# Kernel optimization log

Hardware: AMD Instinct MI355X
Metric: run time of the kernel (lower is better)

## Reference

```python
import jax, jax.numpy as jnp
import numpy as np

D_MODEL = 1024
N_HEADS = 16
HEAD_DIM = D_MODEL // N_HEADS  # 64
SEQ = 2048
BATCH = 2


def setup_inputs() -> dict:
    key = jax.random.key(0)
    ks = jax.random.split(key, 12)
    s = 1.0 / np.sqrt(D_MODEL)
    return {
        "query": jax.random.normal(ks[0], (SEQ, BATCH, D_MODEL), jnp.float32),
        "key": jax.random.normal(ks[1], (SEQ, BATCH, D_MODEL), jnp.float32),
        "value": jax.random.normal(ks[2], (SEQ, BATCH, D_MODEL), jnp.float32),
        "Wq": jax.random.normal(ks[3], (D_MODEL, D_MODEL), jnp.float32) * s,
        "bq": jax.random.normal(ks[4], (D_MODEL,), jnp.float32) * s,
        "Wk": jax.random.normal(ks[5], (D_MODEL, D_MODEL), jnp.float32) * s,
        "bk": jax.random.normal(ks[6], (D_MODEL,), jnp.float32) * s,
        "Wv": jax.random.normal(ks[7], (D_MODEL, D_MODEL), jnp.float32) * s,
        "bv": jax.random.normal(ks[8], (D_MODEL,), jnp.float32) * s,
        "Wo": jax.random.normal(ks[9], (D_MODEL, D_MODEL), jnp.float32) * s,
        "bo": jax.random.normal(ks[10], (D_MODEL,), jnp.float32) * s,
    }


def _rope_tables(seq_len):
    # theta_i = 1 / 10000^(2i/head_dim), i in [0, head_dim//2)
    theta = 1.0 / (10000.0 ** (2.0 * jnp.arange(HEAD_DIM // 2, dtype=jnp.float32) / HEAD_DIM))
    pos = jnp.arange(seq_len, dtype=jnp.float32)[:, None, None, None] * theta  # [S,1,1,hd/2]
    return jnp.sin(pos), jnp.cos(pos)


def _apply_rope(t, sin, cos):
    # t: [S, B, H, hd]; NOTE faithful to source: t2 = q1*sin - q2*cos (minus)
    h = HEAD_DIM // 2
    q1, q2 = t[..., :h], t[..., h:]
    return jnp.concatenate([q1 * cos - q2 * sin, q1 * sin - q2 * cos], axis=-1)


def reference(query, key, value, Wq, bq, Wk, bk, Wv, bv, Wo, bo):
    S, B, _ = query.shape
    q = (query @ Wq.T + bq).reshape(S, B, N_HEADS, HEAD_DIM)
    k = (key @ Wk.T + bk).reshape(S, B, N_HEADS, HEAD_DIM)
    v = (value @ Wv.T + bv).reshape(S, B, N_HEADS, HEAD_DIM)
    sin, cos = _rope_tables(S)
    q = _apply_rope(q, sin, cos)
    k = _apply_rope(k, sin, cos)
    # [S,B,H,d] -> [B,H,S,d]
    q = q.transpose(1, 2, 0, 3)
    k = k.transpose(1, 2, 0, 3)
    v = v.transpose(1, 2, 0, 3)
    scale = 1.0 / jnp.sqrt(jnp.float32(HEAD_DIM))
    scores = jnp.einsum("bhqd,bhkd->bhqk", q, k) * scale
    attn = jax.nn.softmax(scores, axis=-1)
    out = jnp.einsum("bhqk,bhkd->bhqd", attn, v)  # [B,H,S,d]
    out = out.transpose(2, 0, 1, 3).reshape(S, B, D_MODEL)
    return out @ Wo.T + bo
```

## Files before the change

### kernel.cpp

```cpp
#include <hip/hip_runtime.h>
#include <hip/hip_bf16.h>
#include <hip/hip_fp16.h>

#define DMODEL 1024
#define NHEADS 16
#define HDIM   64
#define SEQ    2048
#define BATCH  2
#define MROWS  (SEQ*BATCH)

typedef unsigned int u32;
typedef unsigned short u16;
typedef __attribute__((ext_vector_type(8))) short bfrag;
typedef __attribute__((ext_vector_type(8))) _Float16 hfrag;
typedef __attribute__((ext_vector_type(4))) float f32x4;
typedef __attribute__((ext_vector_type(16))) float f32x16;
typedef union { u32 u[4]; bfrag f; } fragu;
typedef union { u32 u[4]; hfrag f; } fragh;

#define LOG2E 1.44269504088896341f

__device__ __forceinline__ u32 f2bf(float x) {
    unsigned u = __float_as_uint(x);
    return (u + 0x7fffu + ((u >> 16) & 1u)) >> 16;
}
__device__ __forceinline__ float bf2f(u32 h) {
    return __uint_as_float(h << 16);
}
__device__ __forceinline__ u32 pk2bf(float a, float b) {
    __hip_bfloat162 t = __float22bfloat162_rn(make_float2(a, b));
    u32 r;
    __builtin_memcpy(&r, &t, 4);
    return r;
}
__device__ __forceinline__ u32 pkf16(float a, float b) {
#if __has_builtin(__builtin_amdgcn_cvt_pkrtz)
    __fp16 __attribute__((ext_vector_type(2))) t = __builtin_amdgcn_cvt_pkrtz(a, b);
    u32 r;
    __builtin_memcpy(&r, &t, 4);
    return r;
#else
    __half2 t = __floats2half2_rn(a, b);
    u32 r;
    __builtin_memcpy(&r, &t, 4);
    return r;
#endif
}
__device__ __forceinline__ float fexp2(float x) {
#if __has_builtin(__builtin_amdgcn_exp2f)
    return __builtin_amdgcn_exp2f(x);
#else
    return exp2f(x);
#endif
}
__device__ __forceinline__ u32 pkhi(u32 u0, u32 u1) {
#if __has_builtin(__builtin_amdgcn_perm)
    return __builtin_amdgcn_perm(u1, u0, 0x07060302u);
#else
    return (u0 >> 16) | (u1 & 0xffff0000u);
#endif
}

__device__ __forceinline__ void gld16(const void* g, void* l) {
    __builtin_amdgcn_global_load_lds(
        (const __attribute__((address_space(1))) unsigned int*)g,
        (__attribute__((address_space(3))) unsigned int*)l, 16, 0, 0);
}


__global__ __launch_bounds__(256) void prep_kernel(
    const float* __restrict__ Wq, const float* __restrict__ Wk,
    const float* __restrict__ Wv, const float* __restrict__ Wo,
    u16* __restrict__ wqb, u16* __restrict__ wkb, u16* __restrict__ wvb,
    u16* __restrict__ wob, float2* __restrict__ tab)
{
    const int y = blockIdx.y;
    if (y == 3) {
        if (blockIdx.x >= 256) return;
        const int e = blockIdx.x * 256 + threadIdx.x;
        const int s = e >> 5, i = e & 31;
        const double th = exp(-(double)i * (9.210340371976184 / 32.0));
        double sn, cs;
        sincos((double)s * th, &sn, &cs);
        tab[e] = make_float2((float)sn, (float)cs);
        return;
    }
    const float* src = (y == 0) ? Wq : (y == 1) ? Wk : (y == 2) ? Wv : Wo;
    u16* dst = (y == 0) ? wqb : (y == 1) ? wkb : (y == 2) ? wvb : wob;
    const bool f16hi = (y < 3);
    const int lane = threadIdx.x & 63;
    const int wv   = threadIdx.x >> 6;
    const int g8   = lane >> 3;
    const int l8   = lane & 7;
    for (int r = 0; r < 2; ++r) {
        const size_t kb = (size_t)blockIdx.x * 8 + (size_t)r * 4 + wv;
        const float4 x4 = *(const float4*)(src + kb * 256 + lane * 4);
        __align__(8) u16 hb[4];
        __align__(8) u16 lb[4];
        const float xs[4] = {x4.x, x4.y, x4.z, x4.w};
        #pragma unroll
        for (int i = 0; i < 4; ++i) {
            if (f16hi) {
                const __half hh = __float2half(xs[i]);
                hb[i] = __half_as_ushort(hh);
                lb[i] = (u16)f2bf(xs[i] - __half2float(hh));
            } else {
                const u32 h = f2bf(xs[i]);
                hb[i] = (u16)h;
                lb[i] = (u16)f2bf(xs[i] - bf2f(h));
            }
        }
        u16* o = dst + kb * 512 + g8 * 64 + l8 * 4;
        *(uint2*)o        = *(const uint2*)hb;
        *(uint2*)(o + 32) = *(const uint2*)lb;
    }
}

__global__ __launch_bounds__(256) void qkv_gemm_kernel(
    const float* __restrict__ query, const float* __restrict__ key,
    const float* __restrict__ value,
    const u16* __restrict__ Wqb, const u16* __restrict__ Wkb,
    const u16* __restrict__ Wvb,
    const float* __restrict__ bq, const float* __restrict__ bk,
    const float* __restrict__ bv, const float2* __restrict__ tab,
    u16* __restrict__ Qh, u16* __restrict__ Ql,
    u16* __restrict__ Kh, u16* __restrict__ Kl,
    u16* __restrict__ VTh)
{
    __shared__ u16 smem16[32768];
    float* sAf = (float*)smem16;
    u16*   sB  = smem16 + 16384;

    const int z  = blockIdx.z;
    const float* Af   = (z == 0) ? query : (z == 1) ? key : value;
    const u16* Wb     = (z == 0) ? Wqb : (z == 1) ? Wkb : Wvb;
    const float* bias = (z == 0) ? bq : (z == 1) ? bk : bv;
    u16* Oh = (z == 0) ? Qh : (z == 1) ? Kh : VTh;
    u16* Ol = (z == 0) ? Ql : (z == 1) ? Kl : nullptr;
    const float rope_scale = (z == 0) ? 0.125f * LOG2E : 1.0f;
    const int mode = (z == 2) ? 1 : 0;

    const int tid   = threadIdx.x;
    const int w     = tid >> 6;
    const int lane  = tid & 63;
    const int lrow  = lane & 15;
    const int lquad = lane >> 4;

    const int id   = blockIdx.x + 16 * blockIdx.y;
    const int xcd  = id & 7;
    const int jj   = id >> 3;
    const int nblk = jj & 7;
    const int mblk = (xcd << 2) | (jj >> 3);
    const int n0   = nblk * 128;
    const int m0   = mblk * 128;

    const int srow8 = lane >> 3;
    const int sch   = (lane & 7) ^ srow8;

    int aoff0[2], aoff1[2];
    #pragma unroll
    for (int mi = 0; mi < 2; ++mi) {
        const int ra = w * 32 + mi * 16 + lrow;
        aoff0[mi] = ra * 32 + (((2 * lquad)     ^ (ra & 7)) << 2);
        aoff1[mi] = ra * 32 + (((2 * lquad + 1) ^ (ra & 7)) << 2);
    }
    int boffh[8], boffl[8];
    #pragma unroll
    for (int ni = 0; ni < 8; ++ni) {
        const int rb = ni * 16 + lrow;
        boffh[ni] = rb * 64 + ((lquad ^ (rb & 7)) << 3);
        boffl[ni] = rb * 64 + (((lquad + 4) ^ (rb & 7)) << 3);
    }

    f32x4 acc[2][8] = {};

    auto stage = [&](int t) {
        const int h = t & 1;
        #pragma unroll
        for (int i = 0; i < 4; ++i) {
            const int slab = w * 4 + i;
            const int row  = slab * 8 + srow8;
            gld16(Af + (size_t)(m0 + row) * 1024 + t * 32 + sch * 4,
                  sAf + h * 4096 + slab * 256);
            gld16(Wb + (size_t)(n0 + row) * 2048 + t * 64 + sch * 8,
                  sB + h * 8192 + slab * 512);
        }
    };

    auto cvtA = [&](const f32x4 a, const f32x4 b, hfrag& a16, bfrag& abf) {
        fragh fh;
        fh.u[0] = pkf16(a[0], a[1]); fh.u[1] = pkf16(a[2], a[3]);
        fh.u[2] = pkf16(b[0], b[1]); fh.u[3] = pkf16(b[2], b[3]);
        fragu fb;
        fb.u[0] = pkhi(__float_as_uint(a[0]), __float_as_uint(a[1]));
        fb.u[1] = pkhi(__float_as_uint(a[2]), __float_as_uint(a[3]));
        fb.u[2] = pkhi(__float_as_uint(b[0]), __float_as_uint(b[1]));
        fb.u[3] = pkhi(__float_as_uint(b[2]), __float_as_uint(b[3]));
        a16 = fh.f; abf = fb.f;
    };

    stage(0);
    for (int t = 0; t < 32; ++t) {
        __syncthreads();
        if (t < 31) stage(t + 1);
        const int h = t & 1;
        const float* sAh_ = sAf + h * 4096;
        const u16*   sBh_ = sB + h * 8192;

        hfrag a16[2];
        bfrag abf[2], bl[8];
        hfrag bh16[8];
        #pragma unroll
        for (int mi = 0; mi < 2; ++mi) {
            const f32x4 a0 = *(const f32x4*)&sAh_[aoff0[mi]];
            const f32x4 a1 = *(const f32x4*)&sAh_[aoff1[mi]];
            cvtA(a0, a1, a16[mi], abf[mi]);
        }
        #pragma unroll
        for (int ni = 0; ni < 8; ++ni) {
            fragh tmp;
            fragu raw;
            raw.f = *(const bfrag*)&sBh_[boffh[ni]];
            tmp.u[0] = raw.u[0]; tmp.u[1] = raw.u[1];
            tmp.u[2] = raw.u[2]; tmp.u[3] = raw.u[3];
            bh16[ni] = tmp.f;
            bl[ni]   = *(const bfrag*)&sBh_[boffl[ni]];
        }

        #pragma unroll
        for (int mi = 0; mi < 2; ++mi)
            #pragma unroll
            for (int ni = 0; ni < 8; ++ni) {
                acc[mi][ni] = __builtin_amdgcn_mfma_f32_16x16x32_f16(a16[mi], bh16[ni], acc[mi][ni], 0, 0, 0);
                acc[mi][ni] = __builtin_amdgcn_mfma_f32_16x16x32_bf16(abf[mi], bl[ni], acc[mi][ni], 0, 0, 0);
            }
    }

    float bn[8];
    #pragma unroll
    for (int ni = 0; ni < 8; ++ni) bn[ni] = bias[n0 + ni * 16 + lrow];

    if (mode == 0) {
        #pragma unroll
        for (int mi = 0; mi < 2; ++mi)
            #pragma unroll
            for (int r = 0; r < 4; ++r) {
                const int mrow = w * 32 + mi * 16 + lquad * 4 + r;
                const int m  = m0 + mrow;
                const int bb = m & 1;
                const int sg = m >> 1;
                #pragma unroll
                for (int hh = 0; hh < 2; ++hh) {
                    const int head = nblk * 2 + hh;
                    const size_t ob = (((size_t)(bb * NHEADS + head) * SEQ) + sg) * HDIM;
                    #pragma unroll
                    for (int ni = 0; ni < 2; ++ni) {
                        const int i = ni * 16 + lrow;
                        const float2 sc = tab[(size_t)sg * 32 + i];
                        const float x1 = acc[mi][hh * 4 + ni][r]     + bn[hh * 4 + ni];
                        const float x2 = acc[mi][hh * 4 + ni + 2][r] + bn[hh * 4 + ni + 2];
                        const float o1 = (x1 * sc.y - x2 * sc.x) * rope_scale;
                        const float o2 = (x1 * sc.x - x2 * sc.y) * rope_scale;
                        const u32 h1 = f2bf(o1);
                        const u32 h2 = f2bf(o2);
                        Oh[ob + i]      = (u16)h1;  Ol[ob + i]      = (u16)f2bf(o1 - bf2f(h1));
                        Oh[ob + i + 32] = (u16)h2;  Ol[ob + i + 32] = (u16)f2bf(o2 - bf2f(h2));
                    }
                }
            }
        return;
    }
    __syncthreads();
    u32* vb = (u32*)smem16;
    for (int p = 0; p < 2; ++p) {
        if (p) __syncthreads();
        #pragma unroll
        for (int mi = 0; mi < 2; ++mi)
            #pragma unroll
            for (int r = 0; r < 4; ++r) {
                const int mrow = w * 32 + mi * 16 + lquad * 4 + r;
                const int bb = mrow & 1;
                const int sl = mrow >> 1;
                if (bb == p) {
                    #pragma unroll
                    for (int ni = 0; ni < 8; ++ni) {
                        const int d = ni * 16 + lrow;
                        vb[d * 65 + sl] = f2bf(acc[mi][ni][r] + bn[ni]);
                    }
                }
            }
        __syncthreads();
        #pragma unroll
        for (int rep = 0; rep < 4; ++rep) {
            const int c  = rep * 256 + tid;
            const int dc = c >> 3;
            const int s8 = c & 7;
            __align__(8) u16 hb[8];
            #pragma unroll
            for (int j = 0; j < 8; ++j)
                hb[j] = (u16)vb[dc * 65 + s8 * 8 + j];
            const int head = nblk * 2 + (dc >> 6);
            const int dd   = dc & 63;
            const size_t orow = ((size_t)(p * NHEADS + head) * HDIM + dd) * SEQ + (m0 >> 1);
            const int blk16 = (s8 >> 1) * 16;
            const int off   = (s8 & 1) * 4;
            *(uint2*)&Oh[orow + blk16 + off]     = *(const uint2*)&hb[0];
            *(uint2*)&Oh[orow + blk16 + 8 + off] = *(const uint2*)&hb[4];
        }
    }
}

template <int NI>
__device__ __forceinline__ void gemm_body(
    int id,
    const u16* __restrict__ Ab, const u16* __restrict__ Wb,
    const float* __restrict__ bias, float* __restrict__ Of,
    u16* smem16)
{
    u16* sA = smem16;
    u16* sB = smem16 + 16384;

    const int tid   = threadIdx.x;
    const int w     = tid >> 6;
    const int lane  = tid & 63;
    const int lrow  = lane & 15;
    const int lquad = lane >> 4;

    const int NBLK = 1024 / (NI * 16);
    const int xcd  = id & 7;
    const int jj   = id >> 3;
    const int nblk = jj & (NBLK - 1);
    const int mblk = (xcd << 2) | (jj / NBLK);
    const int n0   = nblk * NI * 16;
    const int m0   = mblk * 128;

    const int srow8 = lane >> 3;
    const int sch   = (lane & 7) ^ srow8;

    int aoffh[2], aoffl[2], boffh[NI], boffl[NI];
    #pragma unroll
    for (int mi = 0; mi < 2; ++mi) {
        const int ra = w * 32 + mi * 16 + lrow;
        aoffh[mi] = ra * 64 + ((lquad ^ (ra & 7)) << 3);
        aoffl[mi] = ra * 64 + (((lquad + 4) ^ (ra & 7)) << 3);
    }
    #pragma unroll
    for (int ni = 0; ni < NI; ++ni) {
        const int rb = ni * 16 + lrow;
        boffh[ni] = rb * 64 + ((lquad ^ (rb & 7)) << 3);
        boffl[ni] = rb * 64 + (((lquad + 4) ^ (rb & 7)) << 3);
    }

    f32x4 acc[2][NI] = {};

    auto stage = [&](int t) {
        const int h = t & 1;
        #pragma unroll
        for (int i = 0; i < 4; ++i) {
            const int slab = w * 4 + i;
            const int row  = slab * 8 + srow8;
            gld16(Ab + (size_t)(m0 + row) * 2048 + t * 64 + sch * 8,
                  sA + h * 8192 + slab * 512);
        }
        #pragma unroll
        for (int i = 0; i < NI / 2; ++i) {
            const int slab = w * (NI / 2) + i;
            const int row  = slab * 8 + srow8;
            gld16(Wb + (size_t)(n0 + row) * 2048 + t * 64 + sch * 8,
                  sB + h * (NI * 1024) + slab * 512);
        }
    };

    stage(0);
    for (int t = 0; t < 32; ++t) {
        __syncthreads();
        if (t < 31) stage(t + 1);
        const int h = t & 1;
        const u16* sAh_ = sA + h * 8192;
        const u16* sBh_ = sB + h * (NI * 1024);

        bfrag ah[2], al[2], bh[NI], bl[NI];
        #pragma unroll
        for (int mi = 0; mi < 2; ++mi) {
            ah[mi] = *(const bfrag*)&sAh_[aoffh[mi]];
            al[mi] = *(const bfrag*)&sAh_[aoffl[mi]];
        }
        #pragma unroll
        for (int ni = 0; ni < NI; ++ni) {
            bh[ni] = *(const bfrag*)&sBh_[boffh[ni]];
            bl[ni] = *(const bfrag*)&sBh_[boffl[ni]];
        }

        #pragma unroll
        for (int mi = 0; mi < 2; ++mi)
            #pragma unroll
            for (int ni = 0; ni < NI; ++ni) {
                acc[mi][ni] = __builtin_amdgcn_mfma_f32_16x16x32_bf16(ah[mi], bh[ni], acc[mi][ni], 0, 0, 0);
                acc[mi][ni] = __builtin_amdgcn_mfma_f32_16x16x32_bf16(ah[mi], bl[ni], acc[mi][ni], 0, 0, 0);
                acc[mi][ni] = __builtin_amdgcn_mfma_f32_16x16x32_bf16(al[mi], bh[ni], acc[mi][ni], 0, 0, 0);
            }
    }

    float bn[NI];
    #pragma unroll
    for (int ni = 0; ni < NI; ++ni) bn[ni] = bias[n0 + ni * 16 + lrow];

    #pragma unroll
    for (int mi = 0; mi < 2; ++mi)
        #pragma unroll
        for (int r = 0; r < 4; ++r) {
            const int m = m0 + w * 32 + mi * 16 + lquad * 4 + r;
            #pragma unroll
            for (int ni = 0; ni < NI; ++ni)
                Of[(size_t)m * 1024 + n0 + ni * 16 + lrow] = acc[mi][ni][r] + bn[ni];
        }
}

__global__ __launch_bounds__(256) void out_gemm_kernel(
    const u16* __restrict__ Ab, const u16* __restrict__ Wb,
    const float* __restrict__ bias, float* __restrict__ Of)
{
    __shared__ u16 smem16[24576];
    const int id = blockIdx.x + 16 * blockIdx.y;
    gemm_body<4>(id, Ab, Wb, bias, Of, smem16);
}

__global__ __launch_bounds__(256) void attn_mfma_kernel(
    const u16* __restrict__ Qh, const u16* __restrict__ Ql,
    const u16* __restrict__ Kh, const u16* __restrict__ Kl,
    const u16* __restrict__ Vh,
    u16* __restrict__ AOb)
{
    __shared__ u16 sKh[8192], sKl[8192];
    __shared__ u16 sVh[8192];

    const int tid  = threadIdx.x;
    const int w    = tid >> 6;
    const int lane = tid & 63;
    const int l31  = lane & 31;
    const int g    = lane >> 5;

    const int id = blockIdx.x + 16 * blockIdx.y;
    const int jj = id >> 3;
    const int bh = ((id & 7) << 2) | (jj >> 4);
    const int qt = jj & 15;

    const size_t qg = ((size_t)bh * SEQ + qt * 128 + w * 32 + l31) * HDIM + g * 8;
    bfrag qfh[4], qfl[4];
    #pragma unroll
    for (int ks = 0; ks < 4; ++ks) {
        qfh[ks] = *(const bfrag*)&Qh[qg + ks * 16];
        qfl[ks] = *(const bfrag*)&Ql[qg + ks * 16];
    }

    const int srow   = lane >> 3;
    const int schunk = (lane & 7) ^ srow;
    const u16* gsrc = nullptr; u16* lbase = nullptr; size_t istep = 0, ktstep = 0;
    if (w == 0) {
        gsrc = Kh + ((size_t)bh * SEQ + srow) * HDIM + schunk * 8;
        istep = 8 * 64; ktstep = 64 * 64; lbase = sKh;
    } else if (w == 1) {
        gsrc = Kl + ((size_t)bh * SEQ + srow) * HDIM + schunk * 8;
        istep = 8 * 64; ktstep = 64 * 64; lbase = sKl;
    } else if (w == 2) {
        gsrc = Vh + ((size_t)bh * HDIM + srow) * SEQ + schunk * 8;
        istep = 8 * SEQ; ktstep = 64; lbase = sVh;
    }

    int koff[2][4];
    #pragma unroll
    for (int a = 0; a < 2; ++a) {
        const int row = a * 32 + l31;
        #pragma unroll
        for (int c = 0; c < 4; ++c)
            koff[a][c] = row * 64 + (((c * 2 + g) ^ (row & 7)) << 3);
    }

    f32x16 accO[2] = {};
    float l_loc = 0.0f;

    auto stage = [&](int kt) {
        if (w < 3) {
            const u16* gp = gsrc + (size_t)kt * ktstep;
            u16* dst = lbase + (kt & 1) * 4096;
            #pragma unroll
            for (int i = 0; i < 8; ++i)
                gld16(gp + (size_t)i * istep, dst + i * 512);
        }
    };

    stage(0);
    for (int kt = 0; kt < SEQ / 64; ++kt) {
        __syncthreads();
        if (kt < SEQ / 64 - 1) stage(kt + 1);
        const int po = (kt & 1) * 4096;

        f32x16 accS[2] = {};
        #pragma unroll
        for (int kg = 0; kg < 2; ++kg)
            #pragma unroll
            for (int ks = 0; ks < 4; ++ks) {
                const bfrag kh_ = *(const bfrag*)&sKh[po + koff[kg][ks]];
                const bfrag kl_ = *(const bfrag*)&sKl[po + koff[kg][ks]];
                accS[kg] = __builtin_amdgcn_mfma_f32_32x32x16_bf16(kh_, qfh[ks], accS[kg], 0, 0, 0);
                accS[kg] = __builtin_amdgcn_mfma_f32_32x32x16_bf16(kh_, qfl[ks], accS[kg], 0, 0, 0);
                accS[kg] = __builtin_amdgcn_mfma_f32_32x32x16_bf16(kl_, qfh[ks], accS[kg], 0, 0, 0);
            }

        float pv[2][16];
        #pragma unroll
        for (int kg = 0; kg < 2; ++kg)
            #pragma unroll
            for (int r = 0; r < 16; ++r) {
                const float p = fexp2(accS[kg][r]);
                pv[kg][r] = p;
                l_loc += p;
            }

        #pragma unroll
        for (int kp = 0; kp < 4; ++kp) {
            const int kg = kp >> 1;
            const int t8 = (kp & 1) * 8;
            fragu ph;
            #pragma unroll
            for (int j2 = 0; j2 < 4; ++j2)
                ph.u[j2] = pk2bf(pv[kg][t8 + 2 * j2], pv[kg][t8 + 2 * j2 + 1]);
            #pragma unroll
            for (int dt = 0; dt < 2; ++dt) {
                const bfrag vh = *(const bfrag*)&sVh[po + koff[dt][kp]];
                accO[dt] = __builtin_amdgcn_mfma_f32_32x32x16_bf16(vh, ph.f, accO[dt], 0, 0, 0);
            }
        }
    }

    const float inv = 1.0f / (l_loc + __shfl_xor(l_loc, 32));

    const int b = bh >> 4;
    const int h = bh & 15;
    const int sg = qt * 128 + w * 32 + l31;
    const int rm = sg * BATCH + b;
    #pragma unroll
    for (int dt = 0; dt < 2; ++dt)
        #pragma unroll
        for (int rq = 0; rq < 4; ++rq) {
            const int j0 = 8 * rq + 4 * g;
            const int t  = h * 2 + dt;
            __align__(8) u16 hb[4];
            __align__(8) u16 lb[4];
            #pragma unroll
            for (int i2 = 0; i2 < 4; ++i2) {
                const float v = accO[dt][rq * 4 + i2] * inv;
                const u32 hh = f2bf(v);
                hb[i2] = (u16)hh;
                lb[i2] = (u16)f2bf(v - bf2f(hh));
            }
            u16* o = AOb + (size_t)rm * 2048 + t * 64 + j0;
            *(uint2*)o        = *(const uint2*)hb;
            *(uint2*)(o + 32) = *(const uint2*)lb;
        }
}

extern "C" void kernel_launch(void* const* d_in, const int* in_sizes, int n_in,
                              void* d_out, int out_size, void* d_ws, size_t ws_size,
                              hipStream_t stream)
{
    const float* query = (const float*)d_in[0];
    const float* key   = (const float*)d_in[1];
    const float* value = (const float*)d_in[2];
    const float* Wq    = (const float*)d_in[3];
    const float* bq    = (const float*)d_in[4];
    const float* Wk    = (const float*)d_in[5];
    const float* bk    = (const float*)d_in[6];
    const float* Wv    = (const float*)d_in[7];
    const float* bv    = (const float*)d_in[8];
    const float* Wo    = (const float*)d_in[9];
    const float* bo    = (const float*)d_in[10];
    float* out = (float*)d_out;

    char* wsb = (char*)d_ws;
    const size_t MB = 1024 * 1024;
    u16* Wqb = (u16*)(wsb + 0 * MB);
    u16* Wkb = (u16*)(wsb + 4 * MB);
    u16* Wvb = (u16*)(wsb + 8 * MB);
    float2* tab = (float2*)(wsb + 12 * MB);
    u16* Qh  = (u16*)(wsb + 16 * MB); u16* Ql  = (u16*)(wsb + 24 * MB);
    u16* Kh  = (u16*)(wsb + 32 * MB); u16* Kl  = (u16*)(wsb + 40 * MB);
    u16* VTh = (u16*)(wsb + 48 * MB);
    u16* Wob = (u16*)(wsb + 56 * MB);
    u16* AOb = (u16*)(wsb + 0 * MB);

    prep_kernel<<<dim3(512, 5), 256, 0, stream>>>(
        Wq, Wk, Wv, Wo, Wqb, Wkb, Wvb, Wob, tab);
    qkv_gemm_kernel<<<dim3(16, 16, 3), 256, 0, stream>>>(
        query, key, value,
        Wqb, Wkb, Wvb, bq, bk, bv, tab, Qh, Ql, Kh, Kl, VTh);
    attn_mfma_kernel<<<dim3(16, 32), 256, 0, stream>>>(
        Qh, Ql, Kh, Kl, VTh, AOb);
    out_gemm_kernel<<<dim3(16, 32), 256, 0, stream>>>(AOb, Wob, bo, out);
}
```

Before: 281.0 us.

## Split attention over two key halves and merge with a combine kernel

The attention kernel now gets a third grid dimension that splits the key sequence into two halves. Each half writes unnormalized fp32 partial outputs and row sums, using the output buffer as scratch for one half. A new combine kernel adds the partials, normalizes, and writes the hi/lo bf16 pair in place for the output GEMM. The aim is to double the number of attention blocks for better CU occupancy and tail balance, at the cost of an extra launch and extra fp32 global memory traffic.

```diff
diff --git a/kernel.cpp b/kernel.cpp
--- a/kernel.cpp
+++ b/kernel.cpp
@@ -429,7 +429,7 @@
     const u16* __restrict__ Qh, const u16* __restrict__ Ql,
     const u16* __restrict__ Kh, const u16* __restrict__ Kl,
     const u16* __restrict__ Vh,
-    u16* __restrict__ AOb)
+    float* __restrict__ O0, float* __restrict__ O1, float* __restrict__ lsum)
 {
     __shared__ u16 sKh[8192], sKl[8192];
     __shared__ u16 sVh[8192];
@@ -439,6 +439,7 @@
     const int lane = tid & 63;
     const int l31  = lane & 31;
     const int g    = lane >> 5;
+    const int z    = blockIdx.z;
 
     const int id = blockIdx.x + 16 * blockIdx.y;
     const int jj = id >> 3;
@@ -489,10 +490,11 @@
         }
     };
 
-    stage(0);
-    for (int kt = 0; kt < SEQ / 64; ++kt) {
+    const int kt0 = z * 16;
+    stage(kt0);
+    for (int kt = kt0; kt < kt0 + 16; ++kt) {
         __syncthreads();
-        if (kt < SEQ / 64 - 1) stage(kt + 1);
+        if (kt < kt0 + 15) stage(kt + 1);
         const int po = (kt & 1) * 4096;
 
         f32x16 accS[2] = {};
@@ -533,31 +535,63 @@
         }
     }
 
-    const float inv = 1.0f / (l_loc + __shfl_xor(l_loc, 32));
+    const float ls = l_loc + __shfl_xor(l_loc, 32);
 
     const int b = bh >> 4;
     const int h = bh & 15;
     const int sg = qt * 128 + w * 32 + l31;
     const int rm = sg * BATCH + b;
+    if (lane < 32)
+        lsum[(size_t)z * 65536 + (size_t)bh * 2048 + sg] = ls;
+    float* Op = z ? O1 : O0;
     #pragma unroll
     for (int dt = 0; dt < 2; ++dt)
         #pragma unroll
         for (int rq = 0; rq < 4; ++rq) {
-            const int j0 = 8 * rq + 4 * g;
-            const int t  = h * 2 + dt;
-            __align__(8) u16 hb[4];
-            __align__(8) u16 lb[4];
-            #pragma unroll
-            for (int i2 = 0; i2 < 4; ++i2) {
-                const float v = accO[dt][rq * 4 + i2] * inv;
-                const u32 hh = f2bf(v);
-                hb[i2] = (u16)hh;
-                lb[i2] = (u16)f2bf(v - bf2f(hh));
-            }
-            u16* o = AOb + (size_t)rm * 2048 + t * 64 + j0;
-            *(uint2*)o        = *(const uint2*)hb;
-            *(uint2*)(o + 32) = *(const uint2*)lb;
-        }
+            float4 v4;
+            v4.x = accO[dt][rq * 4 + 0];
+            v4.y = accO[dt][rq * 4 + 1];
+            v4.z = accO[dt][rq * 4 + 2];
+            v4.w = accO[dt][rq * 4 + 3];
+            *(float4*)&Op[(size_t)rm * 1024 + (h * 2 + dt) * 32 + 8 * rq + 4 * g] = v4;
+        }
+}
+
+__global__ __launch_bounds__(256) void combine_kernel(
+    float* __restrict__ O0, const float* __restrict__ O1,
+    const float* __restrict__ lsum)
+{
+    const int lane = threadIdx.x & 63;
+    const int wv   = threadIdx.x >> 6;
+    const int g8   = lane >> 3;
+    const int l8   = lane & 7;
+    #pragma unroll
+    for (int r = 0; r < 8; ++r) {
+        const size_t kb = (size_t)blockIdx.x * 32 + (size_t)r * 4 + wv;
+        const int rm = (int)(kb >> 2);
+        const int t  = ((int)kb & 3) * 8 + g8;
+        const int b  = rm & 1;
+        const int sg = rm >> 1;
+        const int h  = t >> 1;
+        const float l0 = lsum[(size_t)(b * 16 + h) * 2048 + sg];
+        const float l1 = lsum[65536 + (size_t)(b * 16 + h) * 2048 + sg];
+        const float inv = 1.0f / (l0 + l1);
+        const float4 x0 = *(const float4*)(O0 + kb * 256 + lane * 4);
+        const float4 x1 = *(const float4*)(O1 + kb * 256 + lane * 4);
+        const float xs[4] = {x0.x + x1.x, x0.y + x1.y, x0.z + x1.z, x0.w + x1.w};
+        __align__(8) u16 hb[4];
+        __align__(8) u16 lb[4];
+        #pragma unroll
+        for (int i = 0; i < 4; ++i) {
+            const float v = xs[i] * inv;
+            const u32 hh = f2bf(v);
+            hb[i] = (u16)hh;
+            lb[i] = (u16)f2bf(v - bf2f(hh));
+        }
+        u16* o = (u16*)O0 + kb * 512 + g8 * 64 + l8 * 4;
+        *(uint2*)o        = *(const uint2*)hb;
+        *(uint2*)(o + 32) = *(const uint2*)lb;
+    }
 }
 
 extern "C" void kernel_launch(void* const* d_in, const int* in_sizes, int n_in,
@@ -587,14 +621,17 @@
     u16* Kh  = (u16*)(wsb + 32 * MB); u16* Kl  = (u16*)(wsb + 40 * MB);
     u16* VTh = (u16*)(wsb + 48 * MB);
     u16* Wob = (u16*)(wsb + 56 * MB);
-    u16* AOb = (u16*)(wsb + 0 * MB);
+    float* O0   = (float*)(wsb + 0 * MB);
+    float* O1   = out;
+    float* lsum = (float*)(wsb + 60 * MB);
 
     prep_kernel<<<dim3(512, 5), 256, 0, stream>>>(
         Wq, Wk, Wv, Wo, Wqb, Wkb, Wvb, Wob, tab);
     qkv_gemm_kernel<<<dim3(16, 16, 3), 256, 0, stream>>>(
         query, key, value,
         Wqb, Wkb, Wvb, bq, bk, bv, tab, Qh, Ql, Kh, Kl, VTh);
-    attn_mfma_kernel<<<dim3(16, 32), 256, 0, stream>>>(
-        Qh, Ql, Kh, Kl, VTh, AOb);
-    out_gemm_kernel<<<dim3(16, 32), 256, 0, stream>>>(AOb, Wob, bo, out);
-}
+    attn_mfma_kernel<<<dim3(16, 32, 2), 256, 0, stream>>>(
+        Qh, Ql, Kh, Kl, VTh, O0, O1, lsum);
+    combine_kernel<<<dim3(512), 256, 0, stream>>>(O0, O1, lsum);
+    out_gemm_kernel<<<dim3(16, 32), 256, 0, stream>>>((const u16*)O0, Wob, bo, out);
+}
```

New measurement: 288.4 us. 2.6% more time.

## Use fp16-hi/bf16 split to cut MFMA count in QK^T and output GEMM

Applied to the files above, without the earlier changes.

Switches the Q/K split format to an fp16 high part plus a bf16 residual, and the attention output and Wo weights to an fp16 high part plus a bf16 part. This lets the QK^T and output projection use two MFMAs per tile instead of three. For Q (z==0) the low part becomes a plain bf16 of the value rather than a residual, so one product approximates the cross term. The gemm_body template is also inlined into out_gemm_kernel. This trades some precision (fp16 range and the changed residual scheme) for fewer matrix instructions.

```diff
diff --git a/kernel.cpp b/kernel.cpp
--- a/kernel.cpp
+++ b/kernel.cpp
@@ -15,8 +15,7 @@
 typedef __attribute__((ext_vector_type(8))) _Float16 hfrag;
 typedef __attribute__((ext_vector_type(4))) float f32x4;
 typedef __attribute__((ext_vector_type(16))) float f32x16;
-typedef union { u32 u[4]; bfrag f; } fragu;
-typedef union { u32 u[4]; hfrag f; } fragh;
+typedef union { u32 u[4]; bfrag f; hfrag h; } fragu;
 
 #define LOG2E 1.44269504088896341f
 
@@ -87,7 +86,6 @@
     }
     const float* src = (y == 0) ? Wq : (y == 1) ? Wk : (y == 2) ? Wv : Wo;
     u16* dst = (y == 0) ? wqb : (y == 1) ? wkb : (y == 2) ? wvb : wob;
-    const bool f16hi = (y < 3);
     const int lane = threadIdx.x & 63;
     const int wv   = threadIdx.x >> 6;
     const int g8   = lane >> 3;
@@ -100,15 +98,9 @@
         const float xs[4] = {x4.x, x4.y, x4.z, x4.w};
         #pragma unroll
         for (int i = 0; i < 4; ++i) {
-            if (f16hi) {
-                const __half hh = __float2half(xs[i]);
-                hb[i] = __half_as_ushort(hh);
-                lb[i] = (u16)f2bf(xs[i] - __half2float(hh));
-            } else {
-                const u32 h = f2bf(xs[i]);
-                hb[i] = (u16)h;
-                lb[i] = (u16)f2bf(xs[i] - bf2f(h));
-            }
+            const __half hh = __float2half(xs[i]);
+            hb[i] = __half_as_ushort(hh);
+            lb[i] = (u16)f2bf(xs[i] - __half2float(hh));
         }
         u16* o = dst + kb * 512 + g8 * 64 + l8 * 4;
         *(uint2*)o        = *(const uint2*)hb;
@@ -188,15 +180,14 @@
     };
 
     auto cvtA = [&](const f32x4 a, const f32x4 b, hfrag& a16, bfrag& abf) {
-        fragh fh;
+        fragu fh, fb;
         fh.u[0] = pkf16(a[0], a[1]); fh.u[1] = pkf16(a[2], a[3]);
         fh.u[2] = pkf16(b[0], b[1]); fh.u[3] = pkf16(b[2], b[3]);
-        fragu fb;
         fb.u[0] = pkhi(__float_as_uint(a[0]), __float_as_uint(a[1]));
         fb.u[1] = pkhi(__float_as_uint(a[2]), __float_as_uint(a[3]));
         fb.u[2] = pkhi(__float_as_uint(b[0]), __float_as_uint(b[1]));
         fb.u[3] = pkhi(__float_as_uint(b[2]), __float_as_uint(b[3]));
-        a16 = fh.f; abf = fb.f;
+        a16 = fh.h; abf = fb.f;
     };
 
     stage(0);
@@ -218,12 +209,9 @@
         }
         #pragma unroll
         for (int ni = 0; ni < 8; ++ni) {
-            fragh tmp;
             fragu raw;
             raw.f = *(const bfrag*)&sBh_[boffh[ni]];
-            tmp.u[0] = raw.u[0]; tmp.u[1] = raw.u[1];
-            tmp.u[2] = raw.u[2]; tmp.u[3] = raw.u[3];
-            bh16[ni] = tmp.f;
+            bh16[ni] = raw.h;
             bl[ni]   = *(const bfrag*)&sBh_[boffl[ni]];
         }
 
@@ -261,10 +249,17 @@
                         const float x2 = acc[mi][hh * 4 + ni + 2][r] + bn[hh * 4 + ni + 2];
                         const float o1 = (x1 * sc.y - x2 * sc.x) * rope_scale;
                         const float o2 = (x1 * sc.x - x2 * sc.y) * rope_scale;
-                        const u32 h1 = f2bf(o1);
-                        const u32 h2 = f2bf(o2);
-                        Oh[ob + i]      = (u16)h1;  Ol[ob + i]      = (u16)f2bf(o1 - bf2f(h1));
-                        Oh[ob + i + 32] = (u16)h2;  Ol[ob + i + 32] = (u16)f2bf(o2 - bf2f(h2));
+                        const __half h1 = __float2half(o1);
+                        const __half h2 = __float2half(o2);
+                        Oh[ob + i]      = __half_as_ushort(h1);
+                        Oh[ob + i + 32] = __half_as_ushort(h2);
+                        if (z == 0) {
+                            Ol[ob + i]      = (u16)f2bf(o1);
+                            Ol[ob + i + 32] = (u16)f2bf(o2);
+                        } else {
+                            Ol[ob + i]      = (u16)f2bf(o1 - __half2float(h1));
+                            Ol[ob + i + 32] = (u16)f2bf(o2 - __half2float(h2));
+                        }
                     }
                 }
             }
@@ -310,15 +305,15 @@
     }
 }
 
-template <int NI>
-__device__ __forceinline__ void gemm_body(
-    int id,
+__global__ __launch_bounds__(256) void out_gemm_kernel(
     const u16* __restrict__ Ab, const u16* __restrict__ Wb,
-    const float* __restrict__ bias, float* __restrict__ Of,
-    u16* smem16)
+    const float* __restrict__ bias, float* __restrict__ Of)
 {
+    __shared__ u16 smem16[24576];
     u16* sA = smem16;
     u16* sB = smem16 + 16384;
+
+    const int id = blockIdx.x + 16 * blockIdx.y;
 
     const int tid   = threadIdx.x;
     const int w     = tid >> 6;
@@ -326,18 +321,17 @@
     const int lrow  = lane & 15;
     const int lquad = lane >> 4;
 
-    const int NBLK = 1024 / (NI * 16);
     const int xcd  = id & 7;
     const int jj   = id >> 3;
-    const int nblk = jj & (NBLK - 1);
-    const int mblk = (xcd << 2) | (jj / NBLK);
-    const int n0   = nblk * NI * 16;
+    const int nblk = jj & 15;
+    const int mblk = (xcd << 2) | (jj >> 4);
+    const int n0   = nblk * 64;
     const int m0   = mblk * 128;
 
     const int srow8 = lane >> 3;
     const int sch   = (lane & 7) ^ srow8;
 
-    int aoffh[2], aoffl[2], boffh[NI], boffl[NI];
+    int aoffh[2], aoffl[2], boffh[4], boffl[4];
     #pragma unroll
     for (int mi = 0; mi < 2; ++mi) {
         const int ra = w * 32 + mi * 16 + lrow;
@@ -345,13 +339,13 @@
         aoffl[mi] = ra * 64 + (((lquad + 4) ^ (ra & 7)) << 3);
     }
     #pragma unroll
-    for (int ni = 0; ni < NI; ++ni) {
+    for (int ni = 0; ni < 4; ++ni) {
         const int rb = ni * 16 + lrow;
         boffh[ni] = rb * 64 + ((lquad ^ (rb & 7)) << 3);
         boffl[ni] = rb * 64 + (((lquad + 4) ^ (rb & 7)) << 3);
     }
 
-    f32x4 acc[2][NI] = {};
+    f32x4 acc[2][4] = {};
 
     auto stage = [&](int t) {
         const int h = t & 1;
@@ -363,11 +357,11 @@
                   sA + h * 8192 + slab * 512);
         }
         #pragma unroll
-        for (int i = 0; i < NI / 2; ++i) {
-            const int slab = w * (NI / 2) + i;
+        for (int i = 0; i < 2; ++i) {
+            const int slab = w * 2 + i;
             const int row  = slab * 8 + srow8;
             gld16(Wb + (size_t)(n0 + row) * 2048 + t * 64 + sch * 8,
-                  sB + h * (NI * 1024) + slab * 512);
+                  sB + h * 4096 + slab * 512);
         }
     };
 
@@ -377,33 +371,37 @@
         if (t < 31) stage(t + 1);
         const int h = t & 1;
         const u16* sAh_ = sA + h * 8192;
-        const u16* sBh_ = sB + h * (NI * 1024);
-
-        bfrag ah[2], al[2], bh[NI], bl[NI];
+        const u16* sBh_ = sB + h * 4096;
+
+        hfrag ah16[2], wh16[4];
+        bfrag abf[2], wl[4];
         #pragma unroll
         for (int mi = 0; mi < 2; ++mi) {
-            ah[mi] = *(const bfrag*)&sAh_[aoffh[mi]];
-            al[mi] = *(const bfrag*)&sAh_[aoffl[mi]];
-        }
-        #pragma unroll
-        for (int ni = 0; ni < NI; ++ni) {
-            bh[ni] = *(const bfrag*)&sBh_[boffh[ni]];
-            bl[ni] = *(const bfrag*)&sBh_[boffl[ni]];
+            fragu raw;
+            raw.f = *(const bfrag*)&sAh_[aoffh[mi]];
+            ah16[mi] = raw.h;
+            abf[mi]  = *(const bfrag*)&sAh_[aoffl[mi]];
+        }
+        #pragma unroll
+        for (int ni = 0; ni < 4; ++ni) {
+            fragu raw;
+            raw.f = *(const bfrag*)&sBh_[boffh[ni]];
+            wh16[ni] = raw.h;
+            wl[ni]   = *(const bfrag*)&sBh_[boffl[ni]];
         }
 
         #pragma unroll
         for (int mi = 0; mi < 2; ++mi)
             #pragma unroll
-            for (int ni = 0; ni < NI; ++ni) {
-                acc[mi][ni] = __builtin_amdgcn_mfma_f32_16x16x32_bf16(ah[mi], bh[ni], acc[mi][ni], 0, 0, 0);
-                acc[mi][ni] = __builtin_amdgcn_mfma_f32_16x16x32_bf16(ah[mi], bl[ni], acc[mi][ni], 0, 0, 0);
-                acc[mi][ni] = __builtin_amdgcn_mfma_f32_16x16x32_bf16(al[mi], bh[ni], acc[mi][ni], 0, 0, 0);
-            }
-    }
-
-    float bn[NI];
-    #pragma unroll
-    for (int ni = 0; ni < NI; ++ni) bn[ni] = bias[n0 + ni * 16 + lrow];
+            for (int ni = 0; ni < 4; ++ni) {
+                acc[mi][ni] = __builtin_amdgcn_mfma_f32_16x16x32_f16(ah16[mi], wh16[ni], acc[mi][ni], 0, 0, 0);
+                acc[mi][ni] = __builtin_amdgcn_mfma_f32_16x16x32_bf16(abf[mi], wl[ni], acc[mi][ni], 0, 0, 0);
+            }
+    }
+
+    float bn[4];
+    #pragma unroll
+    for (int ni = 0; ni < 4; ++ni) bn[ni] = bias[n0 + ni * 16 + lrow];
 
     #pragma unroll
     for (int mi = 0; mi < 2; ++mi)
@@ -411,18 +409,9 @@
         for (int r = 0; r < 4; ++r) {
             const int m = m0 + w * 32 + mi * 16 + lquad * 4 + r;
             #pragma unroll
-            for (int ni = 0; ni < NI; ++ni)
+            for (int ni = 0; ni < 4; ++ni)
                 Of[(size_t)m * 1024 + n0 + ni * 16 + lrow] = acc[mi][ni][r] + bn[ni];
         }
-}
-
-__global__ __launch_bounds__(256) void out_gemm_kernel(
-    const u16* __restrict__ Ab, const u16* __restrict__ Wb,
-    const float* __restrict__ bias, float* __restrict__ Of)
-{
-    __shared__ u16 smem16[24576];
-    const int id = blockIdx.x + 16 * blockIdx.y;
-    gemm_body<4>(id, Ab, Wb, bias, Of, smem16);
 }
 
 __global__ __launch_bounds__(256) void attn_mfma_kernel(
@@ -446,11 +435,14 @@
     const int qt = jj & 15;
 
     const size_t qg = ((size_t)bh * SEQ + qt * 128 + w * 32 + l31) * HDIM + g * 8;
-    bfrag qfh[4], qfl[4];
+    hfrag qf16[4];
+    bfrag qbf[4];
     #pragma unroll
     for (int ks = 0; ks < 4; ++ks) {
-        qfh[ks] = *(const bfrag*)&Qh[qg + ks * 16];
-        qfl[ks] = *(const bfrag*)&Ql[qg + ks * 16];
+        fragu raw;
+        raw.f = *(const bfrag*)&Qh[qg + ks * 16];
+        qf16[ks] = raw.h;
+        qbf[ks]  = *(const bfrag*)&Ql[qg + ks * 16];
     }
 
     const int srow   = lane >> 3;
@@ -500,11 +492,11 @@
         for (int kg = 0; kg < 2; ++kg)
             #pragma unroll
             for (int ks = 0; ks < 4; ++ks) {
-                const bfrag kh_ = *(const bfrag*)&sKh[po + koff[kg][ks]];
-                const bfrag kl_ = *(const bfrag*)&sKl[po + koff[kg][ks]];
-                accS[kg] = __builtin_amdgcn_mfma_f32_32x32x16_bf16(kh_, qfh[ks], accS[kg], 0, 0, 0);
-                accS[kg] = __builtin_amdgcn_mfma_f32_32x32x16_bf16(kh_, qfl[ks], accS[kg], 0, 0, 0);
-                accS[kg] = __builtin_amdgcn_mfma_f32_32x32x16_bf16(kl_, qfh[ks], accS[kg], 0, 0, 0);
+                fragu kraw;
+                kraw.f = *(const bfrag*)&sKh[po + koff[kg][ks]];
+                const bfrag kres = *(const bfrag*)&sKl[po + koff[kg][ks]];
+                accS[kg] = __builtin_amdgcn_mfma_f32_32x32x16_f16(kraw.h, qf16[ks], accS[kg], 0, 0, 0);
+                accS[kg] = __builtin_amdgcn_mfma_f32_32x32x16_bf16(kres, qbf[ks], accS[kg], 0, 0, 0);
             }
 
         float pv[2][16];
@@ -545,18 +537,16 @@
         for (int rq = 0; rq < 4; ++rq) {
             const int j0 = 8 * rq + 4 * g;
             const int t  = h * 2 + dt;
-            __align__(8) u16 hb[4];
-            __align__(8) u16 lb[4];
-            #pragma unroll
-            for (int i2 = 0; i2 < 4; ++i2) {
-                const float v = accO[dt][rq * 4 + i2] * inv;
-                const u32 hh = f2bf(v);
-                hb[i2] = (u16)hh;
-                lb[i2] = (u16)f2bf(v - bf2f(hh));
-            }
+            float v0 = accO[dt][rq * 4 + 0] * inv;
+            float v1 = accO[dt][rq * 4 + 1] * inv;
+            float v2 = accO[dt][rq * 4 + 2] * inv;
+            float v3 = accO[dt][rq * 4 + 3] * inv;
+            uint2 hbu, lbu;
+            hbu.x = pkf16(v0, v1); hbu.y = pkf16(v2, v3);
+            lbu.x = pk2bf(v0, v1); lbu.y = pk2bf(v2, v3);
             u16* o = AOb + (size_t)rm * 2048 + t * 64 + j0;
-            *(uint2*)o        = *(const uint2*)hb;
-            *(uint2*)(o + 32) = *(const uint2*)lb;
+            *(uint2*)o        = hbu;
+            *(uint2*)(o + 32) = lbu;
         }
 }
 
```

Result: no change. 281.8 us (+0.3%).
